# Kernel tuning notes

Measured on AMD Instinct MI355X. Metric: run time of the kernel, lower is better.

Reference implementation:

```python
import jax, jax.numpy as jnp
import numpy as np

EPS = 1e-8
B, L, D = 8, 2048, 128

def _l2norm(x):
    # F.normalize-style: x / max(||x||, eps)
    n = jnp.sqrt(jnp.sum(x * x, axis=-1, keepdims=True))
    return x / jnp.maximum(n, EPS)

def setup_inputs() -> dict:
    key = jax.random.key(0)
    k0, k1, k2, k3, k4 = jax.random.split(key, 5)
    context = jax.random.normal(k0, (B, 2, L, D), dtype=jnp.float32)
    # MlpModule (BLINK-style): Linear(D, D) -> ReLU -> Linear(D, 1)
    W1 = jax.random.normal(k1, (D, D), dtype=jnp.float32) * (1.0 / np.sqrt(D))
    b1 = jnp.zeros((D,), dtype=jnp.float32)
    W2 = jax.random.normal(k2, (D, 1), dtype=jnp.float32) * (1.0 / np.sqrt(D))
    b2 = jnp.zeros((1,), dtype=jnp.float32)
    return {"context": context, "W1": W1, "b1": b1, "W2": W2, "b2": b2}

def reference(context, W1, b1, W2, b2):
    ctx = context[:, 0]          # [B, L, D] mention-side tokens
    ent = context[:, 1]          # [B, L, D] entity-side tokens
    cn = _l2norm(ctx)
    en = _l2norm(ent)
    # cosine similarity matrix [B, L, L]
    sim = jnp.einsum("bld,bmd->blm", cn, en)
    idx = jnp.argmax(sim, axis=-1)                          # [B, L]
    matched = jnp.take_along_axis(en, idx[..., None], axis=1)  # [B, L, D]
    pair = jnp.stack([cn, matched], axis=-2)                # [B, L, 2, D]
    h = jax.nn.relu(pair @ W1 + b1)                         # [B, L, 2, D]
    out = h @ W2 + b2                                       # [B, L, 2, 1]
    return jnp.sum(out, axis=-2).squeeze(-1)                # [B, L]
```

## Files before the change

### kernel.cpp

```cpp
#include <hip/hip_runtime.h>
#include <hip/hip_bf16.h>

#define B_ 8
#define L_ 2048
#define D_ 128
#define BL_ (B_ * L_)
#define DELTA2 0.016f
#define QCAP 4096

typedef __attribute__((ext_vector_type(8))) short bf16x8;
typedef __attribute__((ext_vector_type(4))) float f32x4;

__device__ __forceinline__ void gload_lds16(const void* g, void* l) {
    __builtin_amdgcn_global_load_lds(
        (const __attribute__((address_space(1))) unsigned int*)g,
        (__attribute__((address_space(3))) unsigned int*)l, 16, 0, 0);
}

#define WAIT_VM(N) asm volatile("s_waitcnt vmcnt(" #N ")" ::: "memory")

__global__ void k_norm(const float* __restrict__ ctx,
                       float* __restrict__ cn, float* __restrict__ en,
                       ushort* __restrict__ cnb, ushort* __restrict__ enb) {
    int wid  = blockIdx.x * 4 + (threadIdx.x >> 6);
    int lane = threadIdx.x & 63;
    int b   = wid >> 12;
    int rem = wid & 4095;
    int c   = rem >> 11;
    int l   = rem & 2047;

    const float* src = ctx + (size_t)wid * D_;
    float2 v = ((const float2*)src)[lane];
    float ss = v.x * v.x + v.y * v.y;
    #pragma unroll
    for (int off = 32; off; off >>= 1) ss += __shfl_down(ss, off, 64);
    ss = __shfl(ss, 0, 64);
    float n = fmaxf(sqrtf(ss), 1e-8f);
    float ox = v.x / n, oy = v.y / n;

    size_t ro = (size_t)(b * L_ + l) * D_;
    float* dst = (c == 0 ? cn : en) + ro;
    ((float2*)dst)[lane] = make_float2(ox, oy);

    __hip_bfloat16 hx = __float2bfloat16(ox), hy = __float2bfloat16(oy);
    ushort ux = *(ushort*)&hx, uy = *(ushort*)&hy;
    ushort* dstb = (c == 0 ? cnb : enb) + ro;
    ((ushort2*)dstb)[lane] = make_ushort2(ux, uy);
}

__global__ __launch_bounds__(512, 2) void k_sim(const ushort* __restrict__ cnb,
                                                const ushort* __restrict__ enb,
                                                const float* __restrict__ cn,
                                                const float* __restrict__ en,
                                                int* __restrict__ finalidx) {
    __shared__ __align__(16) char Bsm[8][4][4096];
    __shared__ float wrowmax[8][64];
    __shared__ float rowth_l[64];
    __shared__ unsigned long long best[64];
    __shared__ int qbuf[QCAP];
    __shared__ int qn;

    const int bid = blockIdx.x;
    const int b = bid & 7, rb = bid >> 3;
    const int row0 = rb * 64;
    const int tid = threadIdx.x;
    const int wave = tid >> 6, lane = tid & 63;
    const int m = lane & 15, q = lane >> 4;

    if (tid == 0) qn = 0;
    if (tid < 64) best[tid] = 0ULL;

    const ushort* Ab = cnb + ((size_t)(b * L_) + row0) * D_;
    const char* gw = (const char*)(enb + (size_t)(b * L_) * D_) + (size_t)wave * 65536;
    char* Bw = &Bsm[wave][0][0];

    bf16x8 Areg[16];
    #pragma unroll
    for (int rt = 0; rt < 4; ++rt)
        #pragma unroll
        for (int kc = 0; kc < 4; ++kc)
            Areg[rt * 4 + kc] = *(const bf16x8*)(Ab + (size_t)(rt * 16 + m) * D_ + kc * 32 + q * 8);

    auto STAGE = [&](int c) {
        const char* gc = gw + (size_t)c * 4096;
        char* lbuf = Bw + (c & 3) * 4096;
        #pragma unroll
        for (int i = 0; i < 4; ++i) {
            int j = i * 4 + q;
            int so = j * 256 + ((m ^ (j & 7)) << 4);
            gload_lds16(gc + so, lbuf + i * 1024);
        }
    };
    auto TILE = [&](int c, f32x4 acc[4]) {
        const char* lbuf = Bw + (c & 3) * 4096;
        #pragma unroll
        for (int rt = 0; rt < 4; ++rt) acc[rt] = (f32x4){0.f, 0.f, 0.f, 0.f};
        #pragma unroll
        for (int kc = 0; kc < 4; ++kc) {
            bf16x8 bf = *(const bf16x8*)(lbuf + m * 256 + ((kc * 64 + q * 16) ^ ((m & 7) << 4)));
            #pragma unroll
            for (int rt = 0; rt < 4; ++rt)
                acc[rt] = __builtin_amdgcn_mfma_f32_16x16x32_bf16(Areg[rt * 4 + kc], bf, acc[rt], 0, 0, 0);
        }
    };

    float runmax[16];
    #pragma unroll
    for (int s = 0; s < 16; ++s) runmax[s] = -3.0e38f;

    auto FMAX = [&](const f32x4 acc[4]) {
        #pragma unroll
        for (int rt = 0; rt < 4; ++rt)
            #pragma unroll
            for (int reg = 0; reg < 4; ++reg)
                runmax[rt * 4 + reg] = fmaxf(runmax[rt * 4 + reg], acc[rt][reg]);
    };

    STAGE(0); STAGE(1); STAGE(2);
    #pragma unroll 1
    for (int c = 0; c < 14; ++c) {
        WAIT_VM(8);
        f32x4 acc[4];
        TILE(c, acc);
        if (c < 13) STAGE(c + 3);
        FMAX(acc);
    }
    { WAIT_VM(4); f32x4 acc[4]; TILE(14, acc); FMAX(acc); }
    { WAIT_VM(0); f32x4 acc[4]; TILE(15, acc); FMAX(acc); }

    #pragma unroll
    for (int s = 0; s < 16; ++s) {
        float v = runmax[s];
        v = fmaxf(v, __shfl_xor(v, 1, 64));
        v = fmaxf(v, __shfl_xor(v, 2, 64));
        v = fmaxf(v, __shfl_xor(v, 4, 64));
        v = fmaxf(v, __shfl_xor(v, 8, 64));
        runmax[s] = v;
    }
    if (m == 0) {
        #pragma unroll
        for (int rt = 0; rt < 4; ++rt)
            #pragma unroll
            for (int reg = 0; reg < 4; ++reg)
                wrowmax[wave][rt * 16 + q * 4 + reg] = runmax[rt * 4 + reg];
    }
    __syncthreads();
    if (tid < 64) {
        float rm = wrowmax[0][tid];
        #pragma unroll
        for (int w = 1; w < 8; ++w) rm = fmaxf(rm, wrowmax[w][tid]);
        rowth_l[tid] = rm - DELTA2;
    }
    __syncthreads();
    float rowth_r[16];
    #pragma unroll
    for (int rt = 0; rt < 4; ++rt)
        #pragma unroll
        for (int reg = 0; reg < 4; ++reg)
            rowth_r[rt * 4 + reg] = rowth_l[rt * 16 + q * 4 + reg];

    auto CAPT = [&](int c, const f32x4 acc[4]) {
        int col = wave * 256 + c * 16 + m;
        #pragma unroll
        for (int rt = 0; rt < 4; ++rt)
            #pragma unroll
            for (int reg = 0; reg < 4; ++reg)
                if (acc[rt][reg] >= rowth_r[rt * 4 + reg]) {
                    int row = rt * 16 + q * 4 + reg;
                    int pos = atomicAdd(&qn, 1);
                    if (pos < QCAP) qbuf[pos] = (row << 12) | col;
                }
    };

    #pragma unroll 1
    for (int d = 0; d < 4; ++d) {
        f32x4 acc[4];
        TILE(15 - d, acc);
        STAGE(11 - d);
        CAPT(15 - d, acc);
    }
    #pragma unroll 1
    for (int d = 4; d < 13; ++d) {
        WAIT_VM(12);
        f32x4 acc[4];
        TILE(15 - d, acc);
        if (d < 12) STAGE(11 - d);
        CAPT(15 - d, acc);
    }
    { WAIT_VM(8); f32x4 acc[4]; TILE(2, acc); CAPT(2, acc); }
    { WAIT_VM(4); f32x4 acc[4]; TILE(1, acc); CAPT(1, acc); }
    { WAIT_VM(0); f32x4 acc[4]; TILE(0, acc); CAPT(0, acc); }
    __syncthreads();

    int qtot = min(qn, QCAP);
    for (int e0 = wave * 4; e0 < qtot; e0 += 32) {
        int e = e0 + q;
        bool act = (e < qtot);
        int pc = qbuf[act ? e : (qtot - 1)];
        int rl = (pc >> 12) & 63, col = pc & 0xFFF;
        const float* ar = cn + ((size_t)(b * L_) + row0 + rl) * D_;
        const float* br = en + ((size_t)(b * L_) + col) * D_;
        float4 x0 = ((const float4*)ar)[m * 2], x1 = ((const float4*)ar)[m * 2 + 1];
        float4 y0 = ((const float4*)br)[m * 2], y1 = ((const float4*)br)[m * 2 + 1];
        double s = (double)x0.x * y0.x + (double)x0.y * y0.y +
                   (double)x0.z * y0.z + (double)x0.w * y0.w +
                   (double)x1.x * y1.x + (double)x1.y * y1.y +
                   (double)x1.z * y1.z + (double)x1.w * y1.w;
        s += __shfl_xor(s, 1, 64);
        s += __shfl_xor(s, 2, 64);
        s += __shfl_xor(s, 4, 64);
        s += __shfl_xor(s, 8, 64);
        if (act && m == 0) {
            unsigned long long ub = (unsigned long long)__double_as_longlong(s);
            ub = (ub & 0x8000000000000000ULL) ? ~ub : (ub | 0x8000000000000000ULL);
            ub = (ub & ~0x7FFULL) | (unsigned long long)(2047 - col);
            atomicMax(&best[rl], ub);
        }
    }
    __syncthreads();
    if (tid < 64)
        finalidx[b * L_ + row0 + tid] = 2047 - (int)(best[tid] & 0x7FFULL);
}

__global__ __launch_bounds__(256) void k_feval(
        const float* __restrict__ X,
        const float* __restrict__ W1, const float* __restrict__ b1,
        const float* __restrict__ W2, const float* __restrict__ b2,
        float* __restrict__ g) {
    __shared__ __align__(16) float As[32][132];
    __shared__ __align__(16) float Bs[32][132];
    __shared__ float redv[128][16];

    int tid = threadIdx.x;
    int tx = tid & 15, ty = tid >> 4;
    int r  = tid >> 3, kg = tid & 7;
    int row0 = blockIdx.x * 128;
    const float* Ab = X + (size_t)row0 * D_;

    float acc[8][8];
    #pragma unroll
    for (int i = 0; i < 8; ++i)
        #pragma unroll
        for (int j = 0; j < 8; ++j) acc[i][j] = 0.0f;

    for (int kc = 0; kc < 4; ++kc) {
        __syncthreads();
        #pragma unroll
        for (int p = 0; p < 4; ++p) {
            int rr = r + 32 * p;
            float4 v = *(const float4*)(Ab + (size_t)rr * D_ + kc * 32 + kg * 4);
            As[kg][rr]      = v.x;
            As[8 + kg][rr]  = v.y;
            As[16 + kg][rr] = v.z;
            As[24 + kg][rr] = v.w;
        }
        {
            int kr = r, phys = (kr & 3) * 8 + (kr >> 2);
            const float* srcp = W1 + (size_t)(kc * 32 + kr) * D_ + kg * 16;
            #pragma unroll
            for (int qq = 0; qq < 4; ++qq)
                *(float4*)&Bs[phys][kg * 16 + qq * 4] = *(const float4*)(srcp + qq * 4);
        }
        __syncthreads();
        #pragma unroll
        for (int k = 0; k < 32; ++k) {
            float a[8], bb[8];
            *(float4*)&a[0]  = *(const float4*)&As[k][ty * 4];
            *(float4*)&a[4]  = *(const float4*)&As[k][64 + ty * 4];
            *(float4*)&bb[0] = *(const float4*)&Bs[k][tx * 4];
            *(float4*)&bb[4] = *(const float4*)&Bs[k][64 + tx * 4];
            #pragma unroll
            for (int i = 0; i < 8; ++i)
                #pragma unroll
                for (int j = 0; j < 8; ++j)
                    acc[i][j] = fmaf(a[i], bb[j], acc[i][j]);
        }
    }

    float w2j[8], b1j[8];
    #pragma unroll
    for (int jj = 0; jj < 8; ++jj) {
        int c = (jj < 4) ? (tx * 4 + jj) : (64 + tx * 4 + (jj - 4));
        w2j[jj] = W2[c];
        b1j[jj] = b1[c];
    }
    float bias2 = b2[0];
    __syncthreads();
    #pragma unroll
    for (int i = 0; i < 8; ++i) {
        float s = 0.0f;
        #pragma unroll
        for (int jj = 0; jj < 8; ++jj)
            s += fmaxf(acc[i][jj] + b1j[jj], 0.0f) * w2j[jj];
        int rowl = (i < 4) ? (ty * 4 + i) : (64 + ty * 4 + (i - 4));
        redv[rowl][tx] = s;
    }
    __syncthreads();
    if (tid < 128) {
        float s = 0.0f;
        #pragma unroll
        for (int tt = 0; tt < 16; ++tt) s += redv[tid][tt];
        g[row0 + tid] = s + bias2;
    }
}

__global__ void k_out(const int* __restrict__ finalidx,
                      const float* __restrict__ g, float* __restrict__ out) {
    int rr = blockIdx.x * 256 + threadIdx.x;
    if (rr >= BL_) return;
    int b = rr >> 11;
    out[rr] = g[rr] + g[BL_ + (b << 11) + finalidx[rr]];
}

extern "C" void kernel_launch(void* const* d_in, const int* in_sizes, int n_in,
                              void* d_out, int out_size, void* d_ws, size_t ws_size,
                              hipStream_t stream) {
    const float* context = (const float*)d_in[0];
    const float* W1 = (const float*)d_in[1];
    const float* b1 = (const float*)d_in[2];
    const float* W2 = (const float*)d_in[3];
    const float* b2 = (const float*)d_in[4];
    float* out = (float*)d_out;

    char* ws = (char*)d_ws;
    float*  cn  = (float*)(ws);
    float*  en  = (float*)(ws + 8388608);
    ushort* cnb = (ushort*)(ws + 16777216);
    ushort* enb = (ushort*)(ws + 20971520);
    float*  g   = (float*)(ws + 25165824);
    int* finalidx = (int*)(ws + 25296896);

    k_norm<<<8192, 256, 0, stream>>>(context, cn, en, cnb, enb);
    k_sim<<<256, 512, 0, stream>>>(cnb, enb, cn, en, finalidx);
    k_feval<<<256, 256, 0, stream>>>(cn, W1, b1, W2, b2, g);
    k_out<<<BL_ / 256, 256, 0, stream>>>(finalidx, g, out);
}
```

Measured before the change: 127.1 us.

## Cache similarity scores in registers and halve rows per block in k_sim

The sim kernel now handles 32 rows per block with twice as many blocks. It loads B tiles straight from global into registers, replacing the swizzled LDS staging via global_load_lds. Each tile's scores are packed to bf16 in registers during the max pass, so the second pass reads those cached values to pick candidates instead of recomputing the MFMA tiles and reloading B. The candidate margin is widened to cover bf16 rounding of the cached scores, which may enqueue more candidates for the fp64 rescoring step.

```diff
diff --git a/kernel.cpp b/kernel.cpp
--- a/kernel.cpp
+++ b/kernel.cpp
@@ -5,19 +5,15 @@
 #define L_ 2048
 #define D_ 128
 #define BL_ (B_ * L_)
-#define DELTA2 0.016f
-#define QCAP 4096
+#define DELTA2W 0.019f
+#define QCAP 2048
+#define ROWS 32
 
 typedef __attribute__((ext_vector_type(8))) short bf16x8;
 typedef __attribute__((ext_vector_type(4))) float f32x4;
 
-__device__ __forceinline__ void gload_lds16(const void* g, void* l) {
-    __builtin_amdgcn_global_load_lds(
-        (const __attribute__((address_space(1))) unsigned int*)g,
-        (__attribute__((address_space(3))) unsigned int*)l, 16, 0, 0);
-}
-
 #define WAIT_VM(N) asm volatile("s_waitcnt vmcnt(" #N ")" ::: "memory")
+#define MFMA(a, bfr, c) __builtin_amdgcn_mfma_f32_16x16x32_bf16(a, bfr, c, 0, 0, 0)
 
 __global__ void k_norm(const float* __restrict__ ctx,
                        float* __restrict__ cn, float* __restrict__ en,
@@ -53,83 +49,82 @@
                                                 const float* __restrict__ cn,
                                                 const float* __restrict__ en,
                                                 int* __restrict__ finalidx) {
-    __shared__ __align__(16) char Bsm[8][4][4096];
-    __shared__ float wrowmax[8][64];
-    __shared__ float rowth_l[64];
-    __shared__ unsigned long long best[64];
+    __shared__ float wrowmax[8][ROWS];
+    __shared__ float rowth_l[ROWS];
+    __shared__ unsigned long long best[ROWS];
     __shared__ int qbuf[QCAP];
     __shared__ int qn;
 
     const int bid = blockIdx.x;
     const int b = bid & 7, rb = bid >> 3;
-    const int row0 = rb * 64;
+    const int row0 = rb * ROWS;
     const int tid = threadIdx.x;
     const int wave = tid >> 6, lane = tid & 63;
     const int m = lane & 15, q = lane >> 4;
 
     if (tid == 0) qn = 0;
-    if (tid < 64) best[tid] = 0ULL;
+    if (tid < ROWS) best[tid] = 0ULL;
 
     const ushort* Ab = cnb + ((size_t)(b * L_) + row0) * D_;
-    const char* gw = (const char*)(enb + (size_t)(b * L_) * D_) + (size_t)wave * 65536;
-    char* Bw = &Bsm[wave][0][0];
-
-    bf16x8 Areg[16];
-    #pragma unroll
-    for (int rt = 0; rt < 4; ++rt)
+    const char*   gw = (const char*)(enb + (size_t)(b * L_) * D_) + (size_t)wave * 65536;
+
+    bf16x8 Areg[8];
+    #pragma unroll
+    for (int rt = 0; rt < 2; ++rt)
         #pragma unroll
         for (int kc = 0; kc < 4; ++kc)
             Areg[rt * 4 + kc] = *(const bf16x8*)(Ab + (size_t)(rt * 16 + m) * D_ + kc * 32 + q * 8);
 
-    auto STAGE = [&](int c) {
-        const char* gc = gw + (size_t)c * 4096;
-        char* lbuf = Bw + (c & 3) * 4096;
-        #pragma unroll
-        for (int i = 0; i < 4; ++i) {
-            int j = i * 4 + q;
-            int so = j * 256 + ((m ^ (j & 7)) << 4);
-            gload_lds16(gc + so, lbuf + i * 1024);
-        }
-    };
-    auto TILE = [&](int c, f32x4 acc[4]) {
-        const char* lbuf = Bw + (c & 3) * 4096;
-        #pragma unroll
-        for (int rt = 0; rt < 4; ++rt) acc[rt] = (f32x4){0.f, 0.f, 0.f, 0.f};
+    bf16x8 bfr[4][4];
+    #pragma unroll
+    for (int c = 0; c < 4; ++c)
+        #pragma unroll
+        for (int kc = 0; kc < 4; ++kc)
+            bfr[c][kc] = *(const bf16x8*)(gw + c * 4096 + m * 256 + kc * 64 + q * 16);
+
+    float runmax[8];
+    #pragma unroll
+    for (int s = 0; s < 8; ++s) runmax[s] = -3.0e38f;
+    unsigned simpk[16][4];
+
+    #pragma unroll
+    for (int c = 0; c < 16; ++c) {
+        if (c <= 12)      WAIT_VM(12);
+        else if (c == 13) WAIT_VM(8);
+        else if (c == 14) WAIT_VM(4);
+        else              WAIT_VM(0);
+
+        f32x4 acc0 = (f32x4){0.f, 0.f, 0.f, 0.f};
+        f32x4 acc1 = (f32x4){0.f, 0.f, 0.f, 0.f};
         #pragma unroll
         for (int kc = 0; kc < 4; ++kc) {
-            bf16x8 bf = *(const bf16x8*)(lbuf + m * 256 + ((kc * 64 + q * 16) ^ ((m & 7) << 4)));
+            acc0 = MFMA(Areg[kc],     bfr[c & 3][kc], acc0);
+            acc1 = MFMA(Areg[4 + kc], bfr[c & 3][kc], acc1);
+        }
+        if (c < 12) {
             #pragma unroll
-            for (int rt = 0; rt < 4; ++rt)
-                acc[rt] = __builtin_amdgcn_mfma_f32_16x16x32_bf16(Areg[rt * 4 + kc], bf, acc[rt], 0, 0, 0);
-        }
-    };
-
-    float runmax[16];
-    #pragma unroll
-    for (int s = 0; s < 16; ++s) runmax[s] = -3.0e38f;
-
-    auto FMAX = [&](const f32x4 acc[4]) {
-        #pragma unroll
-        for (int rt = 0; rt < 4; ++rt)
-            #pragma unroll
-            for (int reg = 0; reg < 4; ++reg)
-                runmax[rt * 4 + reg] = fmaxf(runmax[rt * 4 + reg], acc[rt][reg]);
-    };
-
-    STAGE(0); STAGE(1); STAGE(2);
-    #pragma unroll 1
-    for (int c = 0; c < 14; ++c) {
-        WAIT_VM(8);
-        f32x4 acc[4];
-        TILE(c, acc);
-        if (c < 13) STAGE(c + 3);
-        FMAX(acc);
-    }
-    { WAIT_VM(4); f32x4 acc[4]; TILE(14, acc); FMAX(acc); }
-    { WAIT_VM(0); f32x4 acc[4]; TILE(15, acc); FMAX(acc); }
-
-    #pragma unroll
-    for (int s = 0; s < 16; ++s) {
+            for (int kc = 0; kc < 4; ++kc)
+                bfr[c & 3][kc] = *(const bf16x8*)(gw + (c + 4) * 4096 + m * 256 + kc * 64 + q * 16);
+        }
+        #pragma unroll
+        for (int reg = 0; reg < 4; ++reg) {
+            runmax[reg]     = fmaxf(runmax[reg],     acc0[reg]);
+            runmax[4 + reg] = fmaxf(runmax[4 + reg], acc1[reg]);
+        }
+        {
+            __hip_bfloat16 h0 = __float2bfloat16(acc0[0]), h1 = __float2bfloat16(acc0[1]);
+            __hip_bfloat16 h2 = __float2bfloat16(acc0[2]), h3 = __float2bfloat16(acc0[3]);
+            __hip_bfloat16 h4 = __float2bfloat16(acc1[0]), h5 = __float2bfloat16(acc1[1]);
+            __hip_bfloat16 h6 = __float2bfloat16(acc1[2]), h7 = __float2bfloat16(acc1[3]);
+            simpk[c][0] = (unsigned)*(ushort*)&h0 | ((unsigned)*(ushort*)&h1 << 16);
+            simpk[c][1] = (unsigned)*(ushort*)&h2 | ((unsigned)*(ushort*)&h3 << 16);
+            simpk[c][2] = (unsigned)*(ushort*)&h4 | ((unsigned)*(ushort*)&h5 << 16);
+            simpk[c][3] = (unsigned)*(ushort*)&h6 | ((unsigned)*(ushort*)&h7 << 16);
+        }
+    }
+
+    #pragma unroll
+    for (int s = 0; s < 8; ++s) {
         float v = runmax[s];
         v = fmaxf(v, __shfl_xor(v, 1, 64));
         v = fmaxf(v, __shfl_xor(v, 2, 64));
@@ -139,57 +134,45 @@
     }
     if (m == 0) {
         #pragma unroll
-        for (int rt = 0; rt < 4; ++rt)
+        for (int rt = 0; rt < 2; ++rt)
             #pragma unroll
             for (int reg = 0; reg < 4; ++reg)
                 wrowmax[wave][rt * 16 + q * 4 + reg] = runmax[rt * 4 + reg];
     }
     __syncthreads();
-    if (tid < 64) {
+    if (tid < ROWS) {
         float rm = wrowmax[0][tid];
         #pragma unroll
         for (int w = 1; w < 8; ++w) rm = fmaxf(rm, wrowmax[w][tid]);
-        rowth_l[tid] = rm - DELTA2;
-    }
-    __syncthreads();
-    float rowth_r[16];
-    #pragma unroll
-    for (int rt = 0; rt < 4; ++rt)
+        rowth_l[tid] = rm - DELTA2W;
+    }
+    __syncthreads();
+    float rowth_r[8];
+    #pragma unroll
+    for (int rt = 0; rt < 2; ++rt)
         #pragma unroll
         for (int reg = 0; reg < 4; ++reg)
             rowth_r[rt * 4 + reg] = rowth_l[rt * 16 + q * 4 + reg];
 
-    auto CAPT = [&](int c, const f32x4 acc[4]) {
-        int col = wave * 256 + c * 16 + m;
-        #pragma unroll
-        for (int rt = 0; rt < 4; ++rt)
-            #pragma unroll
-            for (int reg = 0; reg < 4; ++reg)
-                if (acc[rt][reg] >= rowth_r[rt * 4 + reg]) {
-                    int row = rt * 16 + q * 4 + reg;
-                    int pos = atomicAdd(&qn, 1);
-                    if (pos < QCAP) qbuf[pos] = (row << 12) | col;
-                }
-    };
-
-    #pragma unroll 1
-    for (int d = 0; d < 4; ++d) {
-        f32x4 acc[4];
-        TILE(15 - d, acc);
-        STAGE(11 - d);
-        CAPT(15 - d, acc);
-    }
-    #pragma unroll 1
-    for (int d = 4; d < 13; ++d) {
-        WAIT_VM(12);
-        f32x4 acc[4];
-        TILE(15 - d, acc);
-        if (d < 12) STAGE(11 - d);
-        CAPT(15 - d, acc);
-    }
-    { WAIT_VM(8); f32x4 acc[4]; TILE(2, acc); CAPT(2, acc); }
-    { WAIT_VM(4); f32x4 acc[4]; TILE(1, acc); CAPT(1, acc); }
-    { WAIT_VM(0); f32x4 acc[4]; TILE(0, acc); CAPT(0, acc); }
+    #pragma unroll
+    for (int c = 0; c < 16; ++c) {
+        int colc = wave * 256 + c * 16 + m;
+        #pragma unroll
+        for (int h = 0; h < 4; ++h) {
+            unsigned pk = simpk[c][h];
+            float v0 = __uint_as_float(pk << 16);
+            float v1 = __uint_as_float(pk & 0xFFFF0000u);
+            int rt = h >> 1, pr = (h & 1) * 2;
+            if (v0 >= rowth_r[rt * 4 + pr]) {
+                int pos = atomicAdd(&qn, 1);
+                if (pos < QCAP) qbuf[pos] = ((rt * 16 + q * 4 + pr) << 12) | colc;
+            }
+            if (v1 >= rowth_r[rt * 4 + pr + 1]) {
+                int pos = atomicAdd(&qn, 1);
+                if (pos < QCAP) qbuf[pos] = ((rt * 16 + q * 4 + pr + 1) << 12) | colc;
+            }
+        }
+    }
     __syncthreads();
 
     int qtot = min(qn, QCAP);
@@ -197,7 +180,7 @@
         int e = e0 + q;
         bool act = (e < qtot);
         int pc = qbuf[act ? e : (qtot - 1)];
-        int rl = (pc >> 12) & 63, col = pc & 0xFFF;
+        int rl = (pc >> 12) & 31, col = pc & 0xFFF;
         const float* ar = cn + ((size_t)(b * L_) + row0 + rl) * D_;
         const float* br = en + ((size_t)(b * L_) + col) * D_;
         float4 x0 = ((const float4*)ar)[m * 2], x1 = ((const float4*)ar)[m * 2 + 1];
@@ -218,7 +201,7 @@
         }
     }
     __syncthreads();
-    if (tid < 64)
+    if (tid < ROWS)
         finalidx[b * L_ + row0 + tid] = 2047 - (int)(best[tid] & 0x7FFULL);
 }
 
@@ -331,7 +314,7 @@
     int* finalidx = (int*)(ws + 25296896);
 
     k_norm<<<8192, 256, 0, stream>>>(context, cn, en, cnb, enb);
-    k_sim<<<256, 512, 0, stream>>>(cnb, enb, cn, en, finalidx);
+    k_sim<<<512, 512, 0, stream>>>(cnb, enb, cn, en, finalidx);
     k_feval<<<256, 256, 0, stream>>>(cn, W1, b1, W2, b2, g);
     k_out<<<BL_ / 256, 256, 0, stream>>>(finalidx, g, out);
 }
```

Measured after the change: 145.5 us. 14.5% more time.

## Fuse MLP with gathered matched rows and output sum into one kernel

Applied to the files above, without the earlier changes.

The MLP kernel previously ran over all cn and en rows (2*B*L rows) and a separate kernel then summed g for each row with g at the argmax index. Now each block takes 64 cn rows plus the 64 en rows picked by finalidx, runs the MLP on them and writes the output directly. This drops the separate output kernel, the g buffer and the MLP pass over unmatched en rows. The block order in k_norm is also changed to interleave batches. The gathered en loads are irregular and the block has to wait on finalidx being loaded into shared memory first.

```diff
diff --git a/kernel.cpp b/kernel.cpp
--- a/kernel.cpp
+++ b/kernel.cpp
@@ -22,14 +22,15 @@
 __global__ void k_norm(const float* __restrict__ ctx,
                        float* __restrict__ cn, float* __restrict__ en,
                        ushort* __restrict__ cnb, ushort* __restrict__ enb) {
-    int wid  = blockIdx.x * 4 + (threadIdx.x >> 6);
+    int bid  = blockIdx.x;
+    int b    = bid & 7;
+    int j    = bid >> 3;
+    int idx  = j * 4 + (threadIdx.x >> 6);
     int lane = threadIdx.x & 63;
-    int b   = wid >> 12;
-    int rem = wid & 4095;
-    int c   = rem >> 11;
-    int l   = rem & 2047;
-
-    const float* src = ctx + (size_t)wid * D_;
+    int c    = idx >> 11;
+    int l    = idx & 2047;
+
+    const float* src = ctx + (((size_t)b * 2 + c) * L_ + l) * D_;
     float2 v = ((const float2*)src)[lane];
     float ss = v.x * v.x + v.y * v.y;
     #pragma unroll
@@ -222,20 +223,29 @@
         finalidx[b * L_ + row0 + tid] = 2047 - (int)(best[tid] & 0x7FFULL);
 }
 
-__global__ __launch_bounds__(256) void k_feval(
-        const float* __restrict__ X,
+__global__ __launch_bounds__(256) void k_mlp(
+        const float* __restrict__ cn, const float* __restrict__ en,
+        const int* __restrict__ finalidx,
         const float* __restrict__ W1, const float* __restrict__ b1,
         const float* __restrict__ W2, const float* __restrict__ b2,
-        float* __restrict__ g) {
+        float* __restrict__ out) {
     __shared__ __align__(16) float As[32][132];
     __shared__ __align__(16) float Bs[32][132];
     __shared__ float redv[128][16];
+    __shared__ float sumv[128];
+    __shared__ int fidxs[64];
 
     int tid = threadIdx.x;
     int tx = tid & 15, ty = tid >> 4;
     int r  = tid >> 3, kg = tid & 7;
-    int row0 = blockIdx.x * 128;
-    const float* Ab = X + (size_t)row0 * D_;
+    int bid = blockIdx.x;
+    int b = bid & 7, rb = bid >> 3;
+    int row0 = rb * 64;
+
+    if (tid < 64) fidxs[tid] = finalidx[b * L_ + row0 + tid];
+
+    const float* cnb_ = cn + ((size_t)(b * L_) + row0) * D_;
+    const float* enb_ = en + (size_t)(b * L_) * D_;
 
     float acc[8][8];
     #pragma unroll
@@ -248,7 +258,9 @@
         #pragma unroll
         for (int p = 0; p < 4; ++p) {
             int rr = r + 32 * p;
-            float4 v = *(const float4*)(Ab + (size_t)rr * D_ + kc * 32 + kg * 4);
+            const float* srow = (rr < 64) ? (cnb_ + (size_t)rr * D_)
+                                          : (enb_ + (size_t)fidxs[rr - 64] * D_);
+            float4 v = *(const float4*)(srow + kc * 32 + kg * 4);
             As[kg][rr]      = v.x;
             As[8 + kg][rr]  = v.y;
             As[16 + kg][rr] = v.z;
@@ -300,16 +312,11 @@
         float s = 0.0f;
         #pragma unroll
         for (int tt = 0; tt < 16; ++tt) s += redv[tid][tt];
-        g[row0 + tid] = s + bias2;
-    }
-}
-
-__global__ void k_out(const int* __restrict__ finalidx,
-                      const float* __restrict__ g, float* __restrict__ out) {
-    int rr = blockIdx.x * 256 + threadIdx.x;
-    if (rr >= BL_) return;
-    int b = rr >> 11;
-    out[rr] = g[rr] + g[BL_ + (b << 11) + finalidx[rr]];
+        sumv[tid] = s + bias2;
+    }
+    __syncthreads();
+    if (tid < 64)
+        out[b * L_ + row0 + tid] = sumv[tid] + sumv[64 + tid];
 }
 
 extern "C" void kernel_launch(void* const* d_in, const int* in_sizes, int n_in,
@@ -327,11 +334,9 @@
     float*  en  = (float*)(ws + 8388608);
     ushort* cnb = (ushort*)(ws + 16777216);
     ushort* enb = (ushort*)(ws + 20971520);
-    float*  g   = (float*)(ws + 25165824);
     int* finalidx = (int*)(ws + 25296896);
 
     k_norm<<<8192, 256, 0, stream>>>(context, cn, en, cnb, enb);
     k_sim<<<256, 512, 0, stream>>>(cnb, enb, cn, en, finalidx);
-    k_feval<<<256, 256, 0, stream>>>(cn, W1, b1, W2, b2, g);
-    k_out<<<BL_ / 256, 256, 0, stream>>>(finalidx, g, out);
-}
+    k_mlp<<<256, 256, 0, stream>>>(cn, en, finalidx, W1, b1, W2, b2, out);
+}
```

Result: no change. 129.3 us (+1.7%).

## Fuse similarity argmax, MLP evaluation and output into one kernel

Applied to the files above, without the earlier changes.

Merges k_sim, k_feval and k_out into a single kernel. Each block runs the MLP on its 64 context rows plus the 64 gathered matched entity rows, and writes the summed output directly. The shared-memory ring is cut from 4 to 2 stages and unioned with the MLP tiles, and QCAP is reduced, so four 512-thread blocks can fit per CU under the launch bounds. This removes two launches and the global round trip through g and finalidx. In exchange the prefetch depth is shallower, only 256 blocks are launched, and the smaller candidate buffer raises the risk of overflow.

```diff
diff --git a/kernel.cpp b/kernel.cpp
--- a/kernel.cpp
+++ b/kernel.cpp
@@ -6,7 +6,7 @@
 #define D_ 128
 #define BL_ (B_ * L_)
 #define DELTA2 0.016f
-#define QCAP 4096
+#define QCAP 1536
 
 typedef __attribute__((ext_vector_type(8))) short bf16x8;
 typedef __attribute__((ext_vector_type(4))) float f32x4;
@@ -48,17 +48,28 @@
     ((ushort2*)dstb)[lane] = make_ushort2(ux, uy);
 }
 
-__global__ __launch_bounds__(512, 2) void k_sim(const ushort* __restrict__ cnb,
-                                                const ushort* __restrict__ enb,
-                                                const float* __restrict__ cn,
-                                                const float* __restrict__ en,
-                                                int* __restrict__ finalidx) {
-    __shared__ __align__(16) char Bsm[8][4][4096];
+__global__ __launch_bounds__(512, 4) void k_simmlp(
+        const ushort* __restrict__ cnb, const ushort* __restrict__ enb,
+        const float* __restrict__ cn,  const float* __restrict__ en,
+        const float* __restrict__ W1,  const float* __restrict__ b1,
+        const float* __restrict__ W2,  const float* __restrict__ b2,
+        float* __restrict__ out) {
+    union SMem {
+        char ring[8][2][4096];
+        struct {
+            float As[32][132];
+            float Bs[32][132];
+            float redv[128][16];
+            float sumv[128];
+        } c;
+    };
+    __shared__ __align__(16) SMem sm;
     __shared__ float wrowmax[8][64];
     __shared__ float rowth_l[64];
     __shared__ unsigned long long best[64];
     __shared__ int qbuf[QCAP];
     __shared__ int qn;
+    __shared__ int fidxs[64];
 
     const int bid = blockIdx.x;
     const int b = bid & 7, rb = bid >> 3;
@@ -72,7 +83,7 @@
 
     const ushort* Ab = cnb + ((size_t)(b * L_) + row0) * D_;
     const char* gw = (const char*)(enb + (size_t)(b * L_) * D_) + (size_t)wave * 65536;
-    char* Bw = &Bsm[wave][0][0];
+    char* Bw = &sm.ring[wave][0][0];
 
     bf16x8 Areg[16];
     #pragma unroll
@@ -83,7 +94,7 @@
 
     auto STAGE = [&](int c) {
         const char* gc = gw + (size_t)c * 4096;
-        char* lbuf = Bw + (c & 3) * 4096;
+        char* lbuf = Bw + (c & 1) * 4096;
         #pragma unroll
         for (int i = 0; i < 4; ++i) {
             int j = i * 4 + q;
@@ -92,7 +103,7 @@
         }
     };
     auto TILE = [&](int c, f32x4 acc[4]) {
-        const char* lbuf = Bw + (c & 3) * 4096;
+        const char* lbuf = Bw + (c & 1) * 4096;
         #pragma unroll
         for (int rt = 0; rt < 4; ++rt) acc[rt] = (f32x4){0.f, 0.f, 0.f, 0.f};
         #pragma unroll
@@ -116,13 +127,13 @@
                 runmax[rt * 4 + reg] = fmaxf(runmax[rt * 4 + reg], acc[rt][reg]);
     };
 
-    STAGE(0); STAGE(1); STAGE(2);
+    STAGE(0); STAGE(1);
     #pragma unroll 1
     for (int c = 0; c < 14; ++c) {
-        WAIT_VM(8);
+        WAIT_VM(4);
         f32x4 acc[4];
         TILE(c, acc);
-        if (c < 13) STAGE(c + 3);
+        STAGE(c + 2);
         FMAX(acc);
     }
     { WAIT_VM(4); f32x4 acc[4]; TILE(14, acc); FMAX(acc); }
@@ -172,22 +183,16 @@
                 }
     };
 
+    { f32x4 acc[4]; TILE(15, acc); STAGE(13); CAPT(15, acc); }
+    { f32x4 acc[4]; TILE(14, acc); STAGE(12); CAPT(14, acc); }
     #pragma unroll 1
-    for (int d = 0; d < 4; ++d) {
+    for (int d = 2; d < 14; ++d) {
+        WAIT_VM(4);
         f32x4 acc[4];
         TILE(15 - d, acc);
-        STAGE(11 - d);
+        STAGE(13 - d);
         CAPT(15 - d, acc);
     }
-    #pragma unroll 1
-    for (int d = 4; d < 13; ++d) {
-        WAIT_VM(12);
-        f32x4 acc[4];
-        TILE(15 - d, acc);
-        if (d < 12) STAGE(11 - d);
-        CAPT(15 - d, acc);
-    }
-    { WAIT_VM(8); f32x4 acc[4]; TILE(2, acc); CAPT(2, acc); }
     { WAIT_VM(4); f32x4 acc[4]; TILE(1, acc); CAPT(1, acc); }
     { WAIT_VM(0); f32x4 acc[4]; TILE(0, acc); CAPT(0, acc); }
     __syncthreads();
@@ -218,62 +223,54 @@
         }
     }
     __syncthreads();
-    if (tid < 64)
-        finalidx[b * L_ + row0 + tid] = 2047 - (int)(best[tid] & 0x7FFULL);
-}
-
-__global__ __launch_bounds__(256) void k_feval(
-        const float* __restrict__ X,
-        const float* __restrict__ W1, const float* __restrict__ b1,
-        const float* __restrict__ W2, const float* __restrict__ b2,
-        float* __restrict__ g) {
-    __shared__ __align__(16) float As[32][132];
-    __shared__ __align__(16) float Bs[32][132];
-    __shared__ float redv[128][16];
-
-    int tid = threadIdx.x;
+    if (tid < 64) fidxs[tid] = 2047 - (int)(best[tid] & 0x7FFULL);
+    __syncthreads();
+
+    const float* cnr = cn + ((size_t)(b * L_) + row0) * D_;
+    const float* enr = en + (size_t)(b * L_) * D_;
+
     int tx = tid & 15, ty = tid >> 4;
-    int r  = tid >> 3, kg = tid & 7;
-    int row0 = blockIdx.x * 128;
-    const float* Ab = X + (size_t)row0 * D_;
-
-    float acc[8][8];
-    #pragma unroll
-    for (int i = 0; i < 8; ++i)
-        #pragma unroll
-        for (int j = 0; j < 8; ++j) acc[i][j] = 0.0f;
+    int r4 = tid >> 2, kg4 = tid & 3;
+
+    float ac[4][8];
+    #pragma unroll
+    for (int i = 0; i < 4; ++i)
+        #pragma unroll
+        for (int j = 0; j < 8; ++j) ac[i][j] = 0.0f;
 
     for (int kc = 0; kc < 4; ++kc) {
         __syncthreads();
-        #pragma unroll
-        for (int p = 0; p < 4; ++p) {
-            int rr = r + 32 * p;
-            float4 v = *(const float4*)(Ab + (size_t)rr * D_ + kc * 32 + kg * 4);
-            As[kg][rr]      = v.x;
-            As[8 + kg][rr]  = v.y;
-            As[16 + kg][rr] = v.z;
-            As[24 + kg][rr] = v.w;
-        }
         {
-            int kr = r, phys = (kr & 3) * 8 + (kr >> 2);
-            const float* srcp = W1 + (size_t)(kc * 32 + kr) * D_ + kg * 16;
-            #pragma unroll
-            for (int qq = 0; qq < 4; ++qq)
-                *(float4*)&Bs[phys][kg * 16 + qq * 4] = *(const float4*)(srcp + qq * 4);
+            const float* srow = (r4 < 64) ? (cnr + (size_t)r4 * D_)
+                                          : (enr + (size_t)fidxs[r4 - 64] * D_);
+            #pragma unroll
+            for (int h = 0; h < 2; ++h) {
+                int kg = 2 * kg4 + h;
+                float4 v = *(const float4*)(srow + kc * 32 + kg * 4);
+                sm.c.As[kg][r4]      = v.x;
+                sm.c.As[8 + kg][r4]  = v.y;
+                sm.c.As[16 + kg][r4] = v.z;
+                sm.c.As[24 + kg][r4] = v.w;
+            }
+        }
+        {
+            int kr = ty, phys = (kr & 3) * 8 + (kr >> 2);
+            const float* srcp = W1 + (size_t)(kc * 32 + kr) * D_ + tx * 8;
+            *(float4*)&sm.c.Bs[phys][tx * 8]     = *(const float4*)(srcp);
+            *(float4*)&sm.c.Bs[phys][tx * 8 + 4] = *(const float4*)(srcp + 4);
         }
         __syncthreads();
         #pragma unroll
         for (int k = 0; k < 32; ++k) {
-            float a[8], bb[8];
-            *(float4*)&a[0]  = *(const float4*)&As[k][ty * 4];
-            *(float4*)&a[4]  = *(const float4*)&As[k][64 + ty * 4];
-            *(float4*)&bb[0] = *(const float4*)&Bs[k][tx * 4];
-            *(float4*)&bb[4] = *(const float4*)&Bs[k][64 + tx * 4];
-            #pragma unroll
-            for (int i = 0; i < 8; ++i)
+            float a[4], bb[8];
+            *(float4*)&a[0]  = *(const float4*)&sm.c.As[k][ty * 4];
+            *(float4*)&bb[0] = *(const float4*)&sm.c.Bs[k][tx * 4];
+            *(float4*)&bb[4] = *(const float4*)&sm.c.Bs[k][64 + tx * 4];
+            #pragma unroll
+            for (int i = 0; i < 4; ++i)
                 #pragma unroll
                 for (int j = 0; j < 8; ++j)
-                    acc[i][j] = fmaf(a[i], bb[j], acc[i][j]);
+                    ac[i][j] = fmaf(a[i], bb[j], ac[i][j]);
         }
     }
 
@@ -287,29 +284,23 @@
     float bias2 = b2[0];
     __syncthreads();
     #pragma unroll
-    for (int i = 0; i < 8; ++i) {
+    for (int i = 0; i < 4; ++i) {
         float s = 0.0f;
         #pragma unroll
         for (int jj = 0; jj < 8; ++jj)
-            s += fmaxf(acc[i][jj] + b1j[jj], 0.0f) * w2j[jj];
-        int rowl = (i < 4) ? (ty * 4 + i) : (64 + ty * 4 + (i - 4));
-        redv[rowl][tx] = s;
+            s += fmaxf(ac[i][jj] + b1j[jj], 0.0f) * w2j[jj];
+        sm.c.redv[ty * 4 + i][tx] = s;
     }
     __syncthreads();
     if (tid < 128) {
         float s = 0.0f;
         #pragma unroll
-        for (int tt = 0; tt < 16; ++tt) s += redv[tid][tt];
-        g[row0 + tid] = s + bias2;
-    }
-}
-
-__global__ void k_out(const int* __restrict__ finalidx,
-                      const float* __restrict__ g, float* __restrict__ out) {
-    int rr = blockIdx.x * 256 + threadIdx.x;
-    if (rr >= BL_) return;
-    int b = rr >> 11;
-    out[rr] = g[rr] + g[BL_ + (b << 11) + finalidx[rr]];
+        for (int tt = 0; tt < 16; ++tt) s += sm.c.redv[tid][tt];
+        sm.c.sumv[tid] = s + bias2;
+    }
+    __syncthreads();
+    if (tid < 64)
+        out[b * L_ + row0 + tid] = sm.c.sumv[tid] + sm.c.sumv[64 + tid];
 }
 
 extern "C" void kernel_launch(void* const* d_in, const int* in_sizes, int n_in,
@@ -327,11 +318,7 @@
     float*  en  = (float*)(ws + 8388608);
     ushort* cnb = (ushort*)(ws + 16777216);
     ushort* enb = (ushort*)(ws + 20971520);
-    float*  g   = (float*)(ws + 25165824);
-    int* finalidx = (int*)(ws + 25296896);
 
     k_norm<<<8192, 256, 0, stream>>>(context, cn, en, cnb, enb);
-    k_sim<<<256, 512, 0, stream>>>(cnb, enb, cn, en, finalidx);
-    k_feval<<<256, 256, 0, stream>>>(cn, W1, b1, W2, b2, g);
-    k_out<<<BL_ / 256, 256, 0, stream>>>(finalidx, g, out);
+    k_simmlp<<<256, 512, 0, stream>>>(cnb, enb, cn, en, W1, b1, W2, b2, out);
 }
```

Result: no change. 129.2 us (+1.7%).
